# Performance work log

Measured on AMD Instinct MI355X. Metric: run time of the kernel, lower is better.

The kernel has to match this reference:

```python
import jax, jax.numpy as jnp
import numpy as np

N_VARS = 2048
BATCH = 1024


def encode_input(pos):
    # pos: [n_vars, batch] -> [2*n_vars + 2, batch]
    # row 0 = 0, row 1 = 1, even rows >=2 = pos, odd rows >=3 = 1 - pos
    n = pos.shape[0]
    out = jnp.zeros((2 * n + 2,) + pos.shape[1:], dtype=pos.dtype)
    out = out.at[1].set(1.0)
    out = out.at[2::2].set(pos)
    out = out.at[3::2].set(1.0 - pos)
    return out


def setup_inputs() -> dict:
    key = jax.random.key(0)
    k0, k1, k2, k3, k4 = jax.random.split(key, 5)
    x = jax.random.uniform(k0, (N_VARS, BATCH), dtype=jnp.float32)
    idx0 = jax.random.randint(k1, (32768, 2), 0, 2 * N_VARS + 2, dtype=jnp.int32)
    idx1 = jax.random.randint(k2, (16384, 2), 0, 32768, dtype=jnp.int32)
    idx2 = jax.random.randint(k3, (8192, 2), 0, 16384, dtype=jnp.int32)
    idx3 = jax.random.randint(k4, (4096, 2), 0, 8192, dtype=jnp.int32)
    return {"x": x, "idx0": idx0, "idx1": idx1, "idx2": idx2, "idx3": idx3}


def reference(x, idx0, idx1, idx2, idx3):
    h = encode_input(x)                  # [2*n_vars+2, B]
    h = h[idx0].prod(axis=1)             # ProductLayer: [32768, B]
    h = h[idx1].sum(axis=1)              # SumLayer:     [16384, B]
    h = h[idx2].prod(axis=1)             # ProductLayer: [8192, B]
    h = h[idx3].sum(axis=1)              # SumLayer:     [4096, B]
    return h
```

## Files before the change

kernel.cpp:

```cpp
#include <hip/hip_runtime.h>
#include <hip/hip_fp16.h>

#define BATCH  1024
#define NVARS  2048
#define N_OUT  4096

#define W32BYTES (NVARS * 64)
#define NW32     (BATCH / 32)

typedef float f32x4 __attribute__((ext_vector_type(4)));
typedef unsigned u32x4 __attribute__((ext_vector_type(4)));

__device__ __forceinline__ __half2 u2h2(unsigned u) {
    union { unsigned u; __half2 h; } c; c.u = u; return c.h;
}
__device__ __forceinline__ unsigned h22u(__half2 h) {
    union { unsigned u; __half2 h; } c; c.h = h; return c.u;
}
__device__ __forceinline__ void sel2sc(unsigned sel, unsigned& s, unsigned& c) {
    c = (sel & 1u) ? 0x3C003C00u : 0u;
    s = (sel == 2u) ? 0x3C003C00u : (sel == 3u) ? 0xBC00BC00u : 0u;
}

__global__ __launch_bounds__(256) void prep_kernel(
    const float* __restrict__ x,
    const int2* __restrict__ idx0,
    const int2* __restrict__ idx1,
    const int2* __restrict__ idx2,
    const int2* __restrict__ idx3,
    unsigned* __restrict__ T,
    char* __restrict__ xh2)
{
    __shared__ char tile[64 * 272];

    const int bid = blockIdx.x;
    const int tid = threadIdx.x;
    const int rt  = bid >> 3;
    const int ct  = bid & 7;
    const int r0  = rt * 64;

    if (bid < 16) {
        const int i = bid * 256 + tid;
        int2 p3 = idx3[i];
        int n = 0;
        #pragma unroll
        for (int t = 0; t < 2; ++t) {
            int2 p2 = idx2[t ? p3.y : p3.x];
            #pragma unroll
            for (int u = 0; u < 2; ++u) {
                int2 p1 = idx1[u ? p2.y : p2.x];
                #pragma unroll
                for (int v = 0; v < 2; ++v) {
                    int2 p0 = idx0[v ? p1.y : p1.x];
                    unsigned w = 0;
                    #pragma unroll
                    for (int e = 0; e < 2; ++e) {
                        int k = e ? p0.y : p0.x;
                        unsigned code;
                        if (k < 2) code = (unsigned)k << 11;
                        else       code = ((2u + (k & 1)) << 11) | ((unsigned)(k - 2) >> 1);
                        w |= code << (16 * e);
                    }
                    __builtin_nontemporal_store(w, &T[(size_t)i * 8 + n]);
                    ++n;
                }
            }
        }
    }

    {
        const int r_l = tid >> 5;
        const int c4  = tid & 31;
        #pragma unroll
        for (int q = 0; q < 8; ++q) {
            const int rr = q * 8 + r_l;
            float4 v = ((const float4*)x)[(size_t)(r0 + rr) * 256 + ct * 32 + c4];
            unsigned h0 = h22u(__floats2half2_rn(v.x, v.y));
            unsigned h1 = h22u(__floats2half2_rn(v.z, v.w));
            unsigned* p = (unsigned*)(tile + rr * 272 + c4 * 8);
            p[0] = h0; p[1] = h1;
        }
    }
    __syncthreads();

    {
        const int wl = tid & 3;
        const int r2 = tid >> 2;
        #pragma unroll
        for (int g = 0; g < 4; ++g) {
            u32x4 v = *reinterpret_cast<const u32x4*>(tile + r2 * 272 + g * 64 + wl * 16);
            const int w32 = ct * 4 + g;
            __builtin_nontemporal_store(
                v, reinterpret_cast<u32x4*>(
                       xh2 + (size_t)w32 * W32BYTES + (r0 + r2) * 64 + wl * 16));
        }
    }
}

__global__ __launch_bounds__(1024) void knowledge_main(
    const char* __restrict__ xh2,
    const uint4* __restrict__ T4,
    float* __restrict__ out)
{
    __shared__ char lds[131072];

    const int bx   = blockIdx.x;
    const int tid  = threadIdx.x;
    const int xcd  = bx & 7;
    const int slot = bx >> 3;
    const int w    = xcd * 4 + (slot & 3);
    const int chunk= slot >> 2;

    {
        const char* src = xh2 + (size_t)w * W32BYTES;
        #pragma unroll
        for (int it = 0; it < 8; ++it) {
            const int u = it * 1024 + tid;
            *(uint4*)(lds + u * 16) = *(const uint4*)(src + u * 16);
        }
    }
    __syncthreads();

    const int cg  = tid & 3;
    const int ol  = tid >> 2;
    const int cgb = cg * 16;

    int o = chunk * 512 + ol;
    uint4 t0 = T4[(size_t)o * 2];
    uint4 t1 = T4[(size_t)o * 2 + 1];

    #pragma unroll 1
    for (int pass = 0; pass < 2; ++pass) {
        const unsigned tw[8] = {t0.x, t0.y, t0.z, t0.w, t1.x, t1.y, t1.z, t1.w};

        if (pass == 0) {
            t0 = T4[(size_t)(o + 256) * 2];
            t1 = T4[(size_t)(o + 256) * 2 + 1];
        }

        float accf[8];
        #pragma unroll
        for (int k = 0; k < 8; ++k) accf[k] = 0.f;

        #pragma unroll
        for (int a3 = 0; a3 < 2; ++a3) {
            __half2 prod2[4];
            #pragma unroll
            for (int a2 = 0; a2 < 2; ++a2) {
                __half2 sum1[4];
                #pragma unroll
                for (int a1 = 0; a1 < 2; ++a1) {
                    const int m = a3 * 4 + a2 * 2 + a1;
                    const unsigned wv = tw[m];
                    uint4 A = *(const uint4*)(lds + ((wv & 0x7FFu) << 6) + cgb);
                    uint4 B = *(const uint4*)(lds + (((wv >> 16) & 0x7FFu) << 6) + cgb);
                    unsigned sa, ca, sb, cb;
                    sel2sc((wv >> 11) & 3u, sa, ca);
                    sel2sc((wv >> 27) & 3u, sb, cb);
                    const unsigned aw[4] = {A.x, A.y, A.z, A.w};
                    const unsigned bw[4] = {B.x, B.y, B.z, B.w};
                    #pragma unroll
                    for (int k = 0; k < 4; ++k) {
                        __half2 va = __hfma2(u2h2(aw[k]), u2h2(sa), u2h2(ca));
                        __half2 vb = __hfma2(u2h2(bw[k]), u2h2(sb), u2h2(cb));
                        __half2 pr = __hmul2(va, vb);
                        sum1[k] = (a1 == 0) ? pr : __hadd2(sum1[k], pr);
                    }
                }
                #pragma unroll
                for (int k = 0; k < 4; ++k)
                    prod2[k] = (a2 == 0) ? sum1[k] : __hmul2(prod2[k], sum1[k]);
            }
            #pragma unroll
            for (int k = 0; k < 4; ++k) {
                float2 pf = __half22float2(prod2[k]);
                accf[2 * k]     += pf.x;
                accf[2 * k + 1] += pf.y;
            }
        }

        float* dst = out + (size_t)o * BATCH + w * 32 + cg * 8;
        f32x4 o0 = {accf[0], accf[1], accf[2], accf[3]};
        f32x4 o1 = {accf[4], accf[5], accf[6], accf[7]};
        *reinterpret_cast<f32x4*>(dst)     = o0;
        *(reinterpret_cast<f32x4*>(dst) + 1) = o1;

        o += 256;
    }
}

__device__ __forceinline__ float Hval(int k, const float* __restrict__ x, int b) {
    if (k < 2) return (float)k;
    float v = x[((k - 2) >> 1) * BATCH + b];
    return (k & 1) ? 1.0f - v : v;
}

__global__ __launch_bounds__(256) void knowledge_fused_kernel(
    const float* __restrict__ x,
    const int2* __restrict__ idx0,
    const int2* __restrict__ idx1,
    const int2* __restrict__ idx2,
    const int2* __restrict__ idx3,
    float* __restrict__ out)
{
    const int i = blockIdx.x;
    const int b = blockIdx.y * blockDim.x + threadIdx.x;
    const int2 p3 = idx3[i];
    float acc3 = 0.0f;
    #pragma unroll
    for (int t = 0; t < 2; ++t) {
        const int2 p2 = idx2[t ? p3.y : p3.x];
        float prod2 = 1.0f;
        #pragma unroll
        for (int u = 0; u < 2; ++u) {
            const int2 p1 = idx1[u ? p2.y : p2.x];
            float sum1 = 0.0f;
            #pragma unroll
            for (int v = 0; v < 2; ++v) {
                const int2 p0 = idx0[v ? p1.y : p1.x];
                sum1 += Hval(p0.x, x, b) * Hval(p0.y, x, b);
            }
            prod2 *= sum1;
        }
        acc3 += prod2;
    }
    out[(size_t)i * BATCH + b] = acc3;
}

extern "C" void kernel_launch(void* const* d_in, const int* in_sizes, int n_in,
                              void* d_out, int out_size, void* d_ws, size_t ws_size,
                              hipStream_t stream) {
    const float* x    = (const float*)d_in[0];
    const int2*  idx0 = (const int2*)d_in[1];
    const int2*  idx1 = (const int2*)d_in[2];
    const int2*  idx2 = (const int2*)d_in[3];
    const int2*  idx3 = (const int2*)d_in[4];
    float* out = (float*)d_out;

    const size_t t_bytes   = (size_t)N_OUT * 8 * sizeof(unsigned);
    const size_t xh2_bytes = (size_t)NW32 * W32BYTES;
    if (ws_size >= t_bytes + xh2_bytes) {
        unsigned* T   = (unsigned*)d_ws;
        char*     xh2 = (char*)d_ws + t_bytes;
        prep_kernel<<<256, 256, 0, stream>>>(x, idx0, idx1, idx2, idx3, T, xh2);
        knowledge_main<<<256, 1024, 0, stream>>>(xh2, (const uint4*)T, out);
    } else {
        dim3 grid(N_OUT, BATCH / 256);
        knowledge_fused_kernel<<<grid, 256, 0, stream>>>(x, idx0, idx1, idx2, idx3, out);
    }
}
```

Baseline: 19.99 us.

## Split batch into 16-column slabs with swizzled 64KB LDS and 512-thread blocks

Changes the half-precision staging layout from 32-column to 16-column slabs, so each block loads 64KB of LDS instead of 128KB and the grid grows to 512 blocks of 512 threads. LDS rows are XOR-swizzled to spread the random row gathers across banks. The index-table load is hoisted above the LDS fill, and output stores become nontemporal. The aim is higher occupancy, with several blocks resident per CU, and fewer bank conflicts. In exchange each output row's index words are read twice as often and each thread does less work per gather.

```diff
diff --git a/kernel.cpp b/kernel.cpp
--- a/kernel.cpp
+++ b/kernel.cpp
@@ -5,8 +5,8 @@
 #define NVARS  2048
 #define N_OUT  4096
 
-#define W32BYTES (NVARS * 64)
-#define NW32     (BATCH / 32)
+#define W16BYTES (NVARS * 32)
+#define NW16     (BATCH / 16)
 
 typedef float f32x4 __attribute__((ext_vector_type(4)));
 typedef unsigned u32x4 __attribute__((ext_vector_type(4)));
@@ -84,83 +84,90 @@
     __syncthreads();
 
     {
-        const int wl = tid & 3;
-        const int r2 = tid >> 2;
-        #pragma unroll
-        for (int g = 0; g < 4; ++g) {
-            u32x4 v = *reinterpret_cast<const u32x4*>(tile + r2 * 272 + g * 64 + wl * 16);
-            const int w32 = ct * 4 + g;
+        #pragma unroll
+        for (int it = 0; it < 4; ++it) {
+            const int idx = it * 256 + tid;
+            const int q  = idx & 1;
+            const int r2 = (idx >> 1) & 63;
+            const int g  = idx >> 7;
+            u32x4 v = *reinterpret_cast<const u32x4*>(tile + r2 * 272 + g * 32 + q * 16);
+            const int w16 = ct * 8 + g;
             __builtin_nontemporal_store(
                 v, reinterpret_cast<u32x4*>(
-                       xh2 + (size_t)w32 * W32BYTES + (r0 + r2) * 64 + wl * 16));
-        }
-    }
-}
-
-__global__ __launch_bounds__(1024) void knowledge_main(
+                       xh2 + (size_t)w16 * W16BYTES + (r0 + r2) * 32 + q * 16));
+        }
+    }
+}
+
+__global__ __launch_bounds__(512, 4) void knowledge_main(
     const char* __restrict__ xh2,
     const uint4* __restrict__ T4,
     float* __restrict__ out)
 {
-    __shared__ char lds[131072];
-
-    const int bx   = blockIdx.x;
-    const int tid  = threadIdx.x;
-    const int xcd  = bx & 7;
-    const int slot = bx >> 3;
-    const int w    = xcd * 4 + (slot & 3);
-    const int chunk= slot >> 2;
-
-    {
-        const char* src = xh2 + (size_t)w * W32BYTES;
-        #pragma unroll
-        for (int it = 0; it < 8; ++it) {
-            const int u = it * 1024 + tid;
-            *(uint4*)(lds + u * 16) = *(const uint4*)(src + u * 16);
-        }
-    }
-    __syncthreads();
-
-    const int cg  = tid & 3;
-    const int ol  = tid >> 2;
-    const int cgb = cg * 16;
+    __shared__ char lds[65536];
+
+    const int bx    = blockIdx.x;
+    const int tid   = threadIdx.x;
+    const int xcd   = bx & 7;
+    const int slot  = bx >> 3;
+    const int w16   = xcd * 8 + (slot & 7);
+    const int chunk = slot >> 3;
+
+    const int cg = tid & 3;
+    const int ol = tid >> 2;
+    const int cq = (cg >> 1) << 4;
+    const int cd = (cg & 1) << 3;
 
     int o = chunk * 512 + ol;
     uint4 t0 = T4[(size_t)o * 2];
     uint4 t1 = T4[(size_t)o * 2 + 1];
 
+    {
+        const char* src = xh2 + (size_t)w16 * W16BYTES;
+        #pragma unroll
+        for (int it = 0; it < 8; ++it) {
+            const int idx = it * 512 + tid;
+            uint4 v = *(const uint4*)(src + idx * 16);
+            const int r = idx >> 1, q = idx & 1;
+            *(uint4*)(lds + ((r * 32 + q * 16) ^ ((r & 7) << 4))) = v;
+        }
+    }
+    __syncthreads();
+
     #pragma unroll 1
-    for (int pass = 0; pass < 2; ++pass) {
+    for (int pass = 0; pass < 4; ++pass) {
         const unsigned tw[8] = {t0.x, t0.y, t0.z, t0.w, t1.x, t1.y, t1.z, t1.w};
 
-        if (pass == 0) {
-            t0 = T4[(size_t)(o + 256) * 2];
-            t1 = T4[(size_t)(o + 256) * 2 + 1];
-        }
-
-        float accf[8];
-        #pragma unroll
-        for (int k = 0; k < 8; ++k) accf[k] = 0.f;
+        if (pass < 3) {
+            t0 = T4[(size_t)(o + 128) * 2];
+            t1 = T4[(size_t)(o + 128) * 2 + 1];
+        }
+
+        float accf[4];
+        #pragma unroll
+        for (int k = 0; k < 4; ++k) accf[k] = 0.f;
 
         #pragma unroll
         for (int a3 = 0; a3 < 2; ++a3) {
-            __half2 prod2[4];
+            __half2 prod2[2];
             #pragma unroll
             for (int a2 = 0; a2 < 2; ++a2) {
-                __half2 sum1[4];
+                __half2 sum1[2];
                 #pragma unroll
                 for (int a1 = 0; a1 < 2; ++a1) {
                     const int m = a3 * 4 + a2 * 2 + a1;
                     const unsigned wv = tw[m];
-                    uint4 A = *(const uint4*)(lds + ((wv & 0x7FFu) << 6) + cgb);
-                    uint4 B = *(const uint4*)(lds + (((wv >> 16) & 0x7FFu) << 6) + cgb);
+                    const int rA = (int)(wv & 0x7FFu);
+                    const int rB = (int)((wv >> 16) & 0x7FFu);
+                    uint2 A = *(const uint2*)(lds + (((rA * 32 + cq) ^ ((rA & 7) << 4)) + cd));
+                    uint2 B = *(const uint2*)(lds + (((rB * 32 + cq) ^ ((rB & 7) << 4)) + cd));
                     unsigned sa, ca, sb, cb;
                     sel2sc((wv >> 11) & 3u, sa, ca);
                     sel2sc((wv >> 27) & 3u, sb, cb);
-                    const unsigned aw[4] = {A.x, A.y, A.z, A.w};
-                    const unsigned bw[4] = {B.x, B.y, B.z, B.w};
+                    const unsigned aw[2] = {A.x, A.y};
+                    const unsigned bw[2] = {B.x, B.y};
                     #pragma unroll
-                    for (int k = 0; k < 4; ++k) {
+                    for (int k = 0; k < 2; ++k) {
                         __half2 va = __hfma2(u2h2(aw[k]), u2h2(sa), u2h2(ca));
                         __half2 vb = __hfma2(u2h2(bw[k]), u2h2(sb), u2h2(cb));
                         __half2 pr = __hmul2(va, vb);
@@ -168,24 +175,22 @@
                     }
                 }
                 #pragma unroll
-                for (int k = 0; k < 4; ++k)
+                for (int k = 0; k < 2; ++k)
                     prod2[k] = (a2 == 0) ? sum1[k] : __hmul2(prod2[k], sum1[k]);
             }
             #pragma unroll
-            for (int k = 0; k < 4; ++k) {
+            for (int k = 0; k < 2; ++k) {
                 float2 pf = __half22float2(prod2[k]);
                 accf[2 * k]     += pf.x;
                 accf[2 * k + 1] += pf.y;
             }
         }
 
-        float* dst = out + (size_t)o * BATCH + w * 32 + cg * 8;
-        f32x4 o0 = {accf[0], accf[1], accf[2], accf[3]};
-        f32x4 o1 = {accf[4], accf[5], accf[6], accf[7]};
-        *reinterpret_cast<f32x4*>(dst)     = o0;
-        *(reinterpret_cast<f32x4*>(dst) + 1) = o1;
-
-        o += 256;
+        float* dst = out + (size_t)o * BATCH + w16 * 16 + cg * 4;
+        f32x4 ov = {accf[0], accf[1], accf[2], accf[3]};
+        __builtin_nontemporal_store(ov, reinterpret_cast<f32x4*>(dst));
+
+        o += 128;
     }
 }
 
@@ -238,12 +243,12 @@
     float* out = (float*)d_out;
 
     const size_t t_bytes   = (size_t)N_OUT * 8 * sizeof(unsigned);
-    const size_t xh2_bytes = (size_t)NW32 * W32BYTES;
+    const size_t xh2_bytes = (size_t)NW16 * W16BYTES;
     if (ws_size >= t_bytes + xh2_bytes) {
         unsigned* T   = (unsigned*)d_ws;
         char*     xh2 = (char*)d_ws + t_bytes;
         prep_kernel<<<256, 256, 0, stream>>>(x, idx0, idx1, idx2, idx3, T, xh2);
-        knowledge_main<<<256, 1024, 0, stream>>>(xh2, (const uint4*)T, out);
+        knowledge_main<<<512, 512, 0, stream>>>(xh2, (const uint4*)T, out);
     } else {
         dim3 grid(N_OUT, BATCH / 256);
         knowledge_fused_kernel<<<grid, 256, 0, stream>>>(x, idx0, idx1, idx2, idx3, out);
```

Result: slower. 21.94 us (+9.7%).
